# Optimization experiments

Measured on AMD Instinct MI355X. Metric: run time of the kernel, lower is better.

## Reference

```python
import jax, jax.numpy as jnp
import numpy as np

DS = 4  # pooling / upsample factor


def _avg_pool(t, ds):
    B, C, H, W = t.shape
    return t.reshape(B, C, H // ds, ds, W // ds, ds).mean(axis=(3, 5))


def setup_inputs() -> dict:
    key = jax.random.key(0)
    ks = jax.random.split(key, 8)
    B, C, H, W = 8, 512, 128, 128
    Ck = C // 4
    inp = jax.random.normal(ks[0], (B, C, H, W), dtype=jnp.float32)
    c2 = jax.random.normal(ks[1], (B, C, H, W), dtype=jnp.float32)
    # 1x1 conv weights == dense matrices over channel dim (with bias, as nn.Conv2d default)
    Wq = jax.random.normal(ks[2], (Ck, C), dtype=jnp.float32) * 0.02
    bq = jax.random.normal(ks[3], (Ck,), dtype=jnp.float32) * 0.02
    Wk = jax.random.normal(ks[4], (Ck, C), dtype=jnp.float32) * 0.02
    bk = jax.random.normal(ks[5], (Ck,), dtype=jnp.float32) * 0.02
    Wv = jax.random.normal(ks[6], (C, C), dtype=jnp.float32) * 0.02
    bv = jax.random.normal(ks[7], (C,), dtype=jnp.float32) * 0.02
    return {"input": inp, "c2": c2, "Wq": Wq, "bq": bq, "Wk": Wk, "bk": bk, "Wv": Wv, "bv": bv}


def reference(input, c2, Wq, bq, Wk, bk, Wv, bv):
    # Note: the torch module's `gamma` parameter is NOT used in forward; faithful omission.
    x = _avg_pool(input, DS)  # [B,C,h,w]
    y = _avg_pool(c2, DS)
    B, C, h, w = x.shape
    N = h * w
    Ck = Wq.shape[0]
    xf = x.reshape(B, C, N)
    yf = y.reshape(B, C, N)
    q = jnp.einsum('oc,bcn->bon', Wq, xf) + bq[None, :, None]  # [B,Ck,N]
    k = jnp.einsum('oc,bcn->bon', Wk, yf) + bk[None, :, None]  # [B,Ck,N]
    v = jnp.einsum('oc,bcn->bon', Wv, yf) + bv[None, :, None]  # [B,C,N]
    scale = jnp.asarray(Ck, x.dtype) ** -0.5
    energy = jnp.einsum('bon,bom->bnm', q, k) * scale  # [B,N,N] = q^T k
    attn = jax.nn.softmax(energy, axis=-1)
    out = jnp.einsum('bcm,bnm->bcn', v, attn)  # v @ attn^T
    out = out.reshape(B, C, h, w)
    # F.interpolate with default mode='nearest' and size = exact integer multiple -> repeat
    out = jnp.repeat(jnp.repeat(out, DS, axis=2), DS, axis=3)
    return out + c2
```

## Files before the change

### kernel.cpp

```cpp
#include <hip/hip_runtime.h>
#include <stdint.h>
#include <stddef.h>

#define Bn   8
#define Cn   512
#define CKn  128
#define Hn   128
#define Nn   1024
#define HPn  32

typedef float f32x4 __attribute__((ext_vector_type(4)));
typedef short bf16x8 __attribute__((ext_vector_type(8)));

__device__ __forceinline__ uint16_t f2b(float f) {
  uint32_t x = __float_as_uint(f);
  uint32_t r = (x + 0x7FFFu + ((x >> 16) & 1u)) >> 16;
  return (uint16_t)r;
}

__device__ __forceinline__ void gld_lds16(const uint16_t* g, short* lds_base, int lane) {
#if __has_builtin(__builtin_amdgcn_global_load_lds)
  __builtin_amdgcn_global_load_lds(
      (const __attribute__((address_space(1))) void*)g,
      (__attribute__((address_space(3))) void*)lds_base, 16, 0, 0);
#else
  *(bf16x8*)(lds_base + lane * 8) = *(const bf16x8*)g;
#endif
}

__device__ __forceinline__ void stage128x32(const uint16_t* __restrict__ g, int ld,
                                            short* lds, int wave, int lane) {
  const int rin = lane >> 2;
  const int cc  = lane & 3;
#pragma unroll
  for (int s = 0; s < 2; ++s) {
    int i = wave * 2 + s;
    gld_lds16(g + (size_t)(i * 16 + rin) * ld + cc * 8, lds + i * 512, lane);
  }
}

__device__ __forceinline__ void gemm_core(const uint16_t* __restrict__ A,
                                          const uint16_t* __restrict__ Bt,
                                          int ld, int K,
                                          short* As, short* Bs,
                                          f32x4 acc[4][4]) {
  const int tid  = threadIdx.x;
  const int lane = tid & 63;
  const int wave = tid >> 6;
  const int wm = wave >> 1, wn = wave & 1;
  const int quad = lane >> 4, l16 = lane & 15;
  for (int kt = 0; kt < K; kt += 32) {
    __syncthreads();
    stage128x32(A + kt, ld, As, wave, lane);
    stage128x32(Bt + kt, ld, Bs, wave, lane);
    __syncthreads();
    bf16x8 af[4], bfr[4];
#pragma unroll
    for (int i = 0; i < 4; ++i) {
      af[i]  = *(const bf16x8*)(As + (wm * 64 + i * 16 + l16) * 32 + quad * 8);
      bfr[i] = *(const bf16x8*)(Bs + (wn * 64 + i * 16 + l16) * 32 + quad * 8);
    }
#pragma unroll
    for (int i = 0; i < 4; ++i)
#pragma unroll
      for (int j = 0; j < 4; ++j)
        acc[i][j] = __builtin_amdgcn_mfma_f32_16x16x32_bf16(af[i], bfr[j], acc[i][j], 0, 0, 0);
  }
}

#define EPI_VARS \
  const int lane = threadIdx.x & 63; const int wave = threadIdx.x >> 6; \
  const int wm = wave >> 1, wn = wave & 1; \
  const int quad = lane >> 4, l16 = lane & 15;

__global__ __launch_bounds__(256) void wconv_kernel(
    const float* __restrict__ Wq, const float* __restrict__ Wk, const float* __restrict__ Wv,
    uint16_t* __restrict__ Wqb, uint16_t* __restrict__ Wkb, uint16_t* __restrict__ Wvb) {
  int i = blockIdx.x * 256 + threadIdx.x;
  if (i < CKn * Cn) { Wqb[i] = f2b(Wq[i]); Wkb[i] = f2b(Wk[i]); }
  Wvb[i] = f2b(Wv[i]);
}

__global__ __launch_bounds__(1024) void pool_kernel(
    const float* __restrict__ input, const float* __restrict__ c2,
    uint16_t* __restrict__ xT, uint16_t* __restrict__ yT) {
  const int cblk = blockIdx.x, ph = blockIdx.y;
  const int b = blockIdx.z >> 1, src = blockIdx.z & 1;
  const float* in = src ? c2 : input;
  uint16_t* out = src ? yT : xT;
  const int tw = threadIdx.x & 31, tc = threadIdx.x >> 5;
  const int c = cblk * 32 + tc;
  const float* p = in + (((size_t)(b * Cn + c) * Hn) + ph * 4) * Hn + tw * 4;
  float s = 0.f;
#pragma unroll
  for (int r = 0; r < 4; ++r) {
    float4 t = *(const float4*)(p + (size_t)r * Hn);
    s += t.x + t.y + t.z + t.w;
  }
  __shared__ float tile[32][33];
  tile[tw][tc] = s * 0.0625f;
  __syncthreads();
  const int tn = threadIdx.x >> 5, tcc = threadIdx.x & 31;
  out[((size_t)b * Nn + ph * 32 + tn) * Cn + cblk * 32 + tcc] = f2b(tile[tn][tcc]);
}

__global__ __launch_bounds__(256) void qkv_kernel(
    const uint16_t* __restrict__ Wqb, const uint16_t* __restrict__ Wkb, const uint16_t* __restrict__ Wvb,
    const float* __restrict__ bq, const float* __restrict__ bk, const float* __restrict__ bv,
    const uint16_t* __restrict__ xT, const uint16_t* __restrict__ yT,
    uint16_t* __restrict__ qT, uint16_t* __restrict__ kT, uint16_t* __restrict__ vm) {
  __shared__ short As[4096], Bs[4096];
  const int bx = blockIdx.x;
  const int b = bx / 48, r = bx % 48;
  const uint16_t *A, *Bt; const float* bias; int mt, nt, op;
  if (r < 8)       { op = 0; mt = 0;            nt = r;            A = Wqb; Bt = xT; bias = bq; }
  else if (r < 16) { op = 1; mt = 0;            nt = r - 8;        A = Wkb; Bt = yT; bias = bk; }
  else             { op = 2; mt = (r - 16) >> 3; nt = (r - 16) & 7; A = Wvb; Bt = yT; bias = bv; }
  A  += (size_t)mt * 128 * Cn;
  Bt += (size_t)b * Nn * Cn + (size_t)nt * 128 * Cn;
  f32x4 acc[4][4];
#pragma unroll
  for (int i = 0; i < 4; ++i)
#pragma unroll
    for (int j = 0; j < 4; ++j) acc[i][j] = (f32x4)0.f;
  gemm_core(A, Bt, Cn, Cn, As, Bs, acc);
  EPI_VARS;
#pragma unroll
  for (int i = 0; i < 4; ++i)
#pragma unroll
    for (int j = 0; j < 4; ++j)
#pragma unroll
      for (int rg = 0; rg < 4; ++rg) {
        int m = mt * 128 + wm * 64 + i * 16 + quad * 4 + rg;
        int n = nt * 128 + wn * 64 + j * 16 + l16;
        float val = acc[i][j][rg] + bias[m];
        if (op == 2) vm[(size_t)b * Cn * Nn + (size_t)m * Nn + n] = f2b(val);
        else {
          uint16_t* dst = (op == 0) ? qT : kT;
          dst[(size_t)b * Nn * CKn + (size_t)n * CKn + m] = f2b(val);
        }
      }
}

__global__ __launch_bounds__(256) void energy_kernel(
    const uint16_t* __restrict__ qT, const uint16_t* __restrict__ kT,
    float* __restrict__ energy) {
  __shared__ short As[4096], Bs[4096];
  const int bx = blockIdx.x;
  const int b = bx >> 6, r = bx & 63, mt = r >> 3, nt = r & 7;
  const uint16_t* A  = qT + (size_t)b * Nn * CKn + (size_t)mt * 128 * CKn;
  const uint16_t* Bt = kT + (size_t)b * Nn * CKn + (size_t)nt * 128 * CKn;
  f32x4 acc[4][4];
#pragma unroll
  for (int i = 0; i < 4; ++i)
#pragma unroll
    for (int j = 0; j < 4; ++j) acc[i][j] = (f32x4)0.f;
  gemm_core(A, Bt, CKn, CKn, As, Bs, acc);
  EPI_VARS;
  const float scale = 0.08838834764831845f;
#pragma unroll
  for (int i = 0; i < 4; ++i)
#pragma unroll
    for (int j = 0; j < 4; ++j)
#pragma unroll
      for (int rg = 0; rg < 4; ++rg) {
        int n = mt * 128 + wm * 64 + i * 16 + quad * 4 + rg;
        int m = nt * 128 + wn * 64 + j * 16 + l16;
        energy[(size_t)b * Nn * Nn + (size_t)n * Nn + m] = acc[i][j][rg] * scale;
      }
}

__global__ __launch_bounds__(256) void softmax_kernel(
    const float* __restrict__ energy, uint16_t* __restrict__ attn) {
  const size_t row = blockIdx.x;
  const float* e = energy + row * Nn;
  const int t = threadIdx.x;
  float v0[4];
  float mx = -3.4e38f;
#pragma unroll
  for (int i = 0; i < 4; ++i) { v0[i] = e[t + i * 256]; mx = fmaxf(mx, v0[i]); }
#pragma unroll
  for (int off = 32; off; off >>= 1) mx = fmaxf(mx, __shfl_xor(mx, off, 64));
  __shared__ float redm[4], reds[4];
  const int lane = t & 63, wave = t >> 6;
  if (lane == 0) redm[wave] = mx;
  __syncthreads();
  mx = fmaxf(fmaxf(redm[0], redm[1]), fmaxf(redm[2], redm[3]));
  float s = 0.f;
#pragma unroll
  for (int i = 0; i < 4; ++i) { v0[i] = __expf(v0[i] - mx); s += v0[i]; }
#pragma unroll
  for (int off = 32; off; off >>= 1) s += __shfl_xor(s, off, 64);
  if (lane == 0) reds[wave] = s;
  __syncthreads();
  s = reds[0] + reds[1] + reds[2] + reds[3];
  const float inv = 1.f / s;
#pragma unroll
  for (int i = 0; i < 4; ++i) attn[row * Nn + t + i * 256] = f2b(v0[i] * inv);
}

__global__ __launch_bounds__(256) void out_kernel(
    const uint16_t* __restrict__ vm, const uint16_t* __restrict__ attn,
    const float* __restrict__ c2, float* __restrict__ out) {
  __shared__ short As[4096], Bs[4096];
  const int bx = blockIdx.x;
  const int b = bx >> 5, r = bx & 31, mt = r >> 3, nt = r & 7;
  const uint16_t* A  = vm   + (size_t)b * Cn * Nn + (size_t)mt * 128 * Nn;
  const uint16_t* Bt = attn + (size_t)b * Nn * Nn + (size_t)nt * 128 * Nn;
  f32x4 acc[4][4];
#pragma unroll
  for (int i = 0; i < 4; ++i)
#pragma unroll
    for (int j = 0; j < 4; ++j) acc[i][j] = (f32x4)0.f;
  gemm_core(A, Bt, Nn, Nn, As, Bs, acc);
  EPI_VARS;
#pragma unroll
  for (int i = 0; i < 4; ++i)
#pragma unroll
    for (int j = 0; j < 4; ++j)
#pragma unroll
      for (int rg = 0; rg < 4; ++rg) {
        int c = mt * 128 + wm * 64 + i * 16 + quad * 4 + rg;
        int n = nt * 128 + wn * 64 + j * 16 + l16;
        int ph = n >> 5, pw = n & 31;
        float val = acc[i][j][rg];
        size_t base = (((size_t)(b * Cn + c) * Hn) + ph * 4) * Hn + pw * 4;
#pragma unroll
        for (int rr = 0; rr < 4; ++rr) {
          float4 t4 = *(const float4*)(c2 + base + (size_t)rr * Hn);
          t4.x += val; t4.y += val; t4.z += val; t4.w += val;
          *(float4*)(out + base + (size_t)rr * Hn) = t4;
        }
      }
}

extern "C" void kernel_launch(void* const* d_in, const int* in_sizes, int n_in,
                              void* d_out, int out_size, void* d_ws, size_t ws_size,
                              hipStream_t stream) {
  const float* input = (const float*)d_in[0];
  const float* c2    = (const float*)d_in[1];
  const float* Wq    = (const float*)d_in[2];
  const float* bq    = (const float*)d_in[3];
  const float* Wk    = (const float*)d_in[4];
  const float* bk    = (const float*)d_in[5];
  const float* Wv    = (const float*)d_in[6];
  const float* bv    = (const float*)d_in[7];
  float* out = (float*)d_out;
  uint8_t* ws = (uint8_t*)d_ws;

  uint16_t* xT   = (uint16_t*)(ws + 0);
  uint16_t* yT   = (uint16_t*)(ws + 8388608);
  uint16_t* Wqb  = (uint16_t*)(ws + 16777216);
  uint16_t* Wkb  = (uint16_t*)(ws + 16908288);
  uint16_t* Wvb  = (uint16_t*)(ws + 17039360);
  uint16_t* qT   = (uint16_t*)(ws + 17563648);
  uint16_t* kT   = (uint16_t*)(ws + 19660800);
  uint16_t* vm   = (uint16_t*)(ws + 21757952);
  float*    eng  = (float*)   (ws + 30146560);
  uint16_t* attn = (uint16_t*)(ws + 63700992);

  hipLaunchKernelGGL(wconv_kernel, dim3(1024), dim3(256), 0, stream,
                     Wq, Wk, Wv, Wqb, Wkb, Wvb);
  hipLaunchKernelGGL(pool_kernel, dim3(16, 32, 16), dim3(1024), 0, stream,
                     input, c2, xT, yT);
  hipLaunchKernelGGL(qkv_kernel, dim3(384), dim3(256), 0, stream,
                     Wqb, Wkb, Wvb, bq, bk, bv, xT, yT, qT, kT, vm);
  hipLaunchKernelGGL(energy_kernel, dim3(512), dim3(256), 0, stream, qT, kT, eng);
  hipLaunchKernelGGL(softmax_kernel, dim3(8192), dim3(256), 0, stream, eng, attn);
  hipLaunchKernelGGL(out_kernel, dim3(256), dim3(256), 0, stream, vm, attn, c2, out);
}
```

Before: 727.8 us.

## Shrink GEMM tiles to 64x128 and split upsample epilogue into separate kernel

Replaces the 128x128 GEMM tile with a 64x128 tile where each wave owns 16 rows, doubling block counts for the qkv, energy and output GEMMs so more CUs are busy. The output GEMM no longer does the c2 add and 4x nearest upsample in its epilogue. It writes a small fp32 intermediate that a new coalesced elementwise kernel reads to produce the final output. The aim is to fix poor occupancy (256 blocks) and the scattered strided epilogue stores. The cost is reloading the B tile twice as often, lower MFMA reuse per wave, and an extra kernel launch plus an intermediate round trip.

```diff
diff --git a/kernel.cpp b/kernel.cpp
--- a/kernel.cpp
+++ b/kernel.cpp
@@ -7,7 +7,6 @@
 #define CKn  128
 #define Hn   128
 #define Nn   1024
-#define HPn  32
 
 typedef float f32x4 __attribute__((ext_vector_type(4)));
 typedef short bf16x8 __attribute__((ext_vector_type(8)));
@@ -28,49 +27,32 @@
 #endif
 }
 
-__device__ __forceinline__ void stage128x32(const uint16_t* __restrict__ g, int ld,
-                                            short* lds, int wave, int lane) {
-  const int rin = lane >> 2;
-  const int cc  = lane & 3;
-#pragma unroll
-  for (int s = 0; s < 2; ++s) {
-    int i = wave * 2 + s;
-    gld_lds16(g + (size_t)(i * 16 + rin) * ld + cc * 8, lds + i * 512, lane);
-  }
-}
-
-__device__ __forceinline__ void gemm_core(const uint16_t* __restrict__ A,
-                                          const uint16_t* __restrict__ Bt,
-                                          int ld, int K,
-                                          short* As, short* Bs,
-                                          f32x4 acc[4][4]) {
+__device__ __forceinline__ void gemm64x128(const uint16_t* __restrict__ A,
+                                           const uint16_t* __restrict__ Bt,
+                                           int lda, int ldb, int K,
+                                           short* As, short* Bs, f32x4 acc[8]) {
   const int tid  = threadIdx.x;
   const int lane = tid & 63;
   const int wave = tid >> 6;
-  const int wm = wave >> 1, wn = wave & 1;
   const int quad = lane >> 4, l16 = lane & 15;
+  const int rin  = lane >> 2, cc = lane & 3;
   for (int kt = 0; kt < K; kt += 32) {
     __syncthreads();
-    stage128x32(A + kt, ld, As, wave, lane);
-    stage128x32(Bt + kt, ld, Bs, wave, lane);
+    gld_lds16(A + (size_t)(wave * 16 + rin) * lda + kt + cc * 8, As + wave * 512, lane);
+    gld_lds16(Bt + (size_t)(wave * 32 + rin) * ldb + kt + cc * 8, Bs + wave * 1024, lane);
+    gld_lds16(Bt + (size_t)(wave * 32 + 16 + rin) * ldb + kt + cc * 8, Bs + wave * 1024 + 512, lane);
     __syncthreads();
-    bf16x8 af[4], bfr[4];
-#pragma unroll
-    for (int i = 0; i < 4; ++i) {
-      af[i]  = *(const bf16x8*)(As + (wm * 64 + i * 16 + l16) * 32 + quad * 8);
-      bfr[i] = *(const bf16x8*)(Bs + (wn * 64 + i * 16 + l16) * 32 + quad * 8);
-    }
-#pragma unroll
-    for (int i = 0; i < 4; ++i)
-#pragma unroll
-      for (int j = 0; j < 4; ++j)
-        acc[i][j] = __builtin_amdgcn_mfma_f32_16x16x32_bf16(af[i], bfr[j], acc[i][j], 0, 0, 0);
+    bf16x8 af = *(const bf16x8*)(As + (wave * 16 + l16) * 32 + quad * 8);
+#pragma unroll
+    for (int j = 0; j < 8; ++j) {
+      bf16x8 bfr = *(const bf16x8*)(Bs + (j * 16 + l16) * 32 + quad * 8);
+      acc[j] = __builtin_amdgcn_mfma_f32_16x16x32_bf16(af, bfr, acc[j], 0, 0, 0);
+    }
   }
 }
 
 #define EPI_VARS \
   const int lane = threadIdx.x & 63; const int wave = threadIdx.x >> 6; \
-  const int wm = wave >> 1, wn = wave & 1; \
   const int quad = lane >> 4, l16 = lane & 15;
 
 __global__ __launch_bounds__(256) void wconv_kernel(
@@ -109,65 +91,57 @@
     const float* __restrict__ bq, const float* __restrict__ bk, const float* __restrict__ bv,
     const uint16_t* __restrict__ xT, const uint16_t* __restrict__ yT,
     uint16_t* __restrict__ qT, uint16_t* __restrict__ kT, uint16_t* __restrict__ vm) {
-  __shared__ short As[4096], Bs[4096];
+  __shared__ short As[2048], Bs[4096];
   const int bx = blockIdx.x;
-  const int b = bx / 48, r = bx % 48;
-  const uint16_t *A, *Bt; const float* bias; int mt, nt, op;
-  if (r < 8)       { op = 0; mt = 0;            nt = r;            A = Wqb; Bt = xT; bias = bq; }
-  else if (r < 16) { op = 1; mt = 0;            nt = r - 8;        A = Wkb; Bt = yT; bias = bk; }
-  else             { op = 2; mt = (r - 16) >> 3; nt = (r - 16) & 7; A = Wvb; Bt = yT; bias = bv; }
-  A  += (size_t)mt * 128 * Cn;
-  Bt += (size_t)b * Nn * Cn + (size_t)nt * 128 * Cn;
-  f32x4 acc[4][4];
-#pragma unroll
-  for (int i = 0; i < 4; ++i)
-#pragma unroll
-    for (int j = 0; j < 4; ++j) acc[i][j] = (f32x4)0.f;
-  gemm_core(A, Bt, Cn, Cn, As, Bs, acc);
+  const int b = bx / 96, r = bx % 96;
+  const int mt = r >> 3, nt = r & 7;
+  int op, mbase; const uint16_t* A; const float* bias;
+  if (mt < 2)      { op = 0; mbase = mt * 64;       A = Wqb + (size_t)mbase * Cn; bias = bq; }
+  else if (mt < 4) { op = 1; mbase = (mt - 2) * 64; A = Wkb + (size_t)mbase * Cn; bias = bk; }
+  else             { op = 2; mbase = (mt - 4) * 64; A = Wvb + (size_t)mbase * Cn; bias = bv; }
+  const uint16_t* Bt = ((op == 0) ? xT : yT) + (size_t)b * Nn * Cn + (size_t)nt * 128 * Cn;
+  f32x4 acc[8];
+#pragma unroll
+  for (int j = 0; j < 8; ++j) acc[j] = (f32x4)0.f;
+  gemm64x128(A, Bt, Cn, Cn, Cn, As, Bs, acc);
   EPI_VARS;
 #pragma unroll
-  for (int i = 0; i < 4; ++i)
-#pragma unroll
-    for (int j = 0; j < 4; ++j)
-#pragma unroll
-      for (int rg = 0; rg < 4; ++rg) {
-        int m = mt * 128 + wm * 64 + i * 16 + quad * 4 + rg;
-        int n = nt * 128 + wn * 64 + j * 16 + l16;
-        float val = acc[i][j][rg] + bias[m];
-        if (op == 2) vm[(size_t)b * Cn * Nn + (size_t)m * Nn + n] = f2b(val);
-        else {
-          uint16_t* dst = (op == 0) ? qT : kT;
-          dst[(size_t)b * Nn * CKn + (size_t)n * CKn + m] = f2b(val);
-        }
+  for (int j = 0; j < 8; ++j)
+#pragma unroll
+    for (int rg = 0; rg < 4; ++rg) {
+      int m = mbase + wave * 16 + quad * 4 + rg;
+      int n = nt * 128 + j * 16 + l16;
+      float val = acc[j][rg] + bias[m];
+      if (op == 2) vm[(size_t)b * Cn * Nn + (size_t)m * Nn + n] = f2b(val);
+      else {
+        uint16_t* dst = (op == 0) ? qT : kT;
+        dst[(size_t)b * Nn * CKn + (size_t)n * CKn + m] = f2b(val);
       }
+    }
 }
 
 __global__ __launch_bounds__(256) void energy_kernel(
     const uint16_t* __restrict__ qT, const uint16_t* __restrict__ kT,
     float* __restrict__ energy) {
-  __shared__ short As[4096], Bs[4096];
+  __shared__ short As[2048], Bs[4096];
   const int bx = blockIdx.x;
-  const int b = bx >> 6, r = bx & 63, mt = r >> 3, nt = r & 7;
-  const uint16_t* A  = qT + (size_t)b * Nn * CKn + (size_t)mt * 128 * CKn;
+  const int b = bx >> 7, r = bx & 127, mt = r >> 3, nt = r & 7;
+  const uint16_t* A  = qT + (size_t)b * Nn * CKn + (size_t)mt * 64 * CKn;
   const uint16_t* Bt = kT + (size_t)b * Nn * CKn + (size_t)nt * 128 * CKn;
-  f32x4 acc[4][4];
-#pragma unroll
-  for (int i = 0; i < 4; ++i)
-#pragma unroll
-    for (int j = 0; j < 4; ++j) acc[i][j] = (f32x4)0.f;
-  gemm_core(A, Bt, CKn, CKn, As, Bs, acc);
+  f32x4 acc[8];
+#pragma unroll
+  for (int j = 0; j < 8; ++j) acc[j] = (f32x4)0.f;
+  gemm64x128(A, Bt, CKn, CKn, CKn, As, Bs, acc);
   EPI_VARS;
   const float scale = 0.08838834764831845f;
 #pragma unroll
-  for (int i = 0; i < 4; ++i)
-#pragma unroll
-    for (int j = 0; j < 4; ++j)
-#pragma unroll
-      for (int rg = 0; rg < 4; ++rg) {
-        int n = mt * 128 + wm * 64 + i * 16 + quad * 4 + rg;
-        int m = nt * 128 + wn * 64 + j * 16 + l16;
-        energy[(size_t)b * Nn * Nn + (size_t)n * Nn + m] = acc[i][j][rg] * scale;
-      }
+  for (int j = 0; j < 8; ++j)
+#pragma unroll
+    for (int rg = 0; rg < 4; ++rg) {
+      int n = mt * 64 + wave * 16 + quad * 4 + rg;
+      int m = nt * 128 + j * 16 + l16;
+      energy[(size_t)b * Nn * Nn + (size_t)n * Nn + m] = acc[j][rg] * scale;
+    }
 }
 
 __global__ __launch_bounds__(256) void softmax_kernel(
@@ -199,39 +173,42 @@
   for (int i = 0; i < 4; ++i) attn[row * Nn + t + i * 256] = f2b(v0[i] * inv);
 }
 
-__global__ __launch_bounds__(256) void out_kernel(
+__global__ __launch_bounds__(256) void outg_kernel(
     const uint16_t* __restrict__ vm, const uint16_t* __restrict__ attn,
-    const float* __restrict__ c2, float* __restrict__ out) {
-  __shared__ short As[4096], Bs[4096];
+    float* __restrict__ osm) {
+  __shared__ short As[2048], Bs[4096];
   const int bx = blockIdx.x;
-  const int b = bx >> 5, r = bx & 31, mt = r >> 3, nt = r & 7;
-  const uint16_t* A  = vm   + (size_t)b * Cn * Nn + (size_t)mt * 128 * Nn;
+  const int b = bx >> 6, r = bx & 63, mt = r >> 3, nt = r & 7;
+  const uint16_t* A  = vm   + (size_t)b * Cn * Nn + (size_t)mt * 64 * Nn;
   const uint16_t* Bt = attn + (size_t)b * Nn * Nn + (size_t)nt * 128 * Nn;
-  f32x4 acc[4][4];
-#pragma unroll
-  for (int i = 0; i < 4; ++i)
-#pragma unroll
-    for (int j = 0; j < 4; ++j) acc[i][j] = (f32x4)0.f;
-  gemm_core(A, Bt, Nn, Nn, As, Bs, acc);
+  f32x4 acc[8];
+#pragma unroll
+  for (int j = 0; j < 8; ++j) acc[j] = (f32x4)0.f;
+  gemm64x128(A, Bt, Nn, Nn, Nn, As, Bs, acc);
   EPI_VARS;
 #pragma unroll
-  for (int i = 0; i < 4; ++i)
-#pragma unroll
-    for (int j = 0; j < 4; ++j)
-#pragma unroll
-      for (int rg = 0; rg < 4; ++rg) {
-        int c = mt * 128 + wm * 64 + i * 16 + quad * 4 + rg;
-        int n = nt * 128 + wn * 64 + j * 16 + l16;
-        int ph = n >> 5, pw = n & 31;
-        float val = acc[i][j][rg];
-        size_t base = (((size_t)(b * Cn + c) * Hn) + ph * 4) * Hn + pw * 4;
-#pragma unroll
-        for (int rr = 0; rr < 4; ++rr) {
-          float4 t4 = *(const float4*)(c2 + base + (size_t)rr * Hn);
-          t4.x += val; t4.y += val; t4.z += val; t4.w += val;
-          *(float4*)(out + base + (size_t)rr * Hn) = t4;
-        }
-      }
+  for (int j = 0; j < 8; ++j)
+#pragma unroll
+    for (int rg = 0; rg < 4; ++rg) {
+      int c = mt * 64 + wave * 16 + quad * 4 + rg;
+      int n = nt * 128 + j * 16 + l16;
+      osm[(size_t)b * Cn * Nn + (size_t)c * Nn + n] = acc[j][rg];
+    }
+}
+
+__global__ __launch_bounds__(256) void upsample_kernel(
+    const float* __restrict__ osm, const float* __restrict__ c2,
+    float* __restrict__ out) {
+  const int t = blockIdx.x * 256 + threadIdx.x;
+  const int ww4 = t & 31;
+  const int hh  = (t >> 5) & 127;
+  const int cb  = t >> 12;
+  const int n = (hh >> 2) * 32 + ww4;
+  const float val = osm[((size_t)cb << 10) + n];
+  const size_t base = (((size_t)cb * Hn) + hh) * Hn + ww4 * 4;
+  float4 t4 = *(const float4*)(c2 + base);
+  t4.x += val; t4.y += val; t4.z += val; t4.w += val;
+  *(float4*)(out + base) = t4;
 }
 
 extern "C" void kernel_launch(void* const* d_in, const int* in_sizes, int n_in,
@@ -258,14 +235,16 @@
   uint16_t* vm   = (uint16_t*)(ws + 21757952);
   float*    eng  = (float*)   (ws + 30146560);
   uint16_t* attn = (uint16_t*)(ws + 63700992);
+  float*    osm  = eng;
 
   hipLaunchKernelGGL(wconv_kernel, dim3(1024), dim3(256), 0, stream,
                      Wq, Wk, Wv, Wqb, Wkb, Wvb);
   hipLaunchKernelGGL(pool_kernel, dim3(16, 32, 16), dim3(1024), 0, stream,
                      input, c2, xT, yT);
-  hipLaunchKernelGGL(qkv_kernel, dim3(384), dim3(256), 0, stream,
+  hipLaunchKernelGGL(qkv_kernel, dim3(768), dim3(256), 0, stream,
                      Wqb, Wkb, Wvb, bq, bk, bv, xT, yT, qT, kT, vm);
-  hipLaunchKernelGGL(energy_kernel, dim3(512), dim3(256), 0, stream, qT, kT, eng);
+  hipLaunchKernelGGL(energy_kernel, dim3(1024), dim3(256), 0, stream, qT, kT, eng);
   hipLaunchKernelGGL(softmax_kernel, dim3(8192), dim3(256), 0, stream, eng, attn);
-  hipLaunchKernelGGL(out_kernel, dim3(256), dim3(256), 0, stream, vm, attn, c2, out);
-}
+  hipLaunchKernelGGL(outg_kernel, dim3(512), dim3(256), 0, stream, vm, attn, osm);
+  hipLaunchKernelGGL(upsample_kernel, dim3(65536), dim3(256), 0, stream, osm, c2, out);
+}
```

After: 705.5 us. 1.03x faster.
